# Kernel tuning notes

Measured on AMD Instinct MI355X. Metric: run time of the kernel, lower is better.

The kernel has to match this reference:

```python
import jax, jax.numpy as jnp
import numpy as np

H = 16          # n_heads
DH = 128        # head_dim
DR = 64         # rope_dim
DC = DH - DR    # content_dim = 64
THETA = 10000.0
SCALE = 1.0 / np.sqrt(DH)


def _rope_tables(T, dtype):
    inv = 1.0 / (THETA ** (jnp.arange(0, DR, 2, dtype=jnp.float32) / DR))  # [DR/2]
    t = jnp.arange(T, dtype=jnp.float32)
    freqs = jnp.outer(t, inv)  # [T, DR/2]
    return jnp.cos(freqs).astype(dtype), jnp.sin(freqs).astype(dtype)


def _apply_rope(x, cos, sin):
    # x: [B,H,T,DR]; cos/sin: [T,DR/2] broadcast over B,H
    d = x.shape[-1] // 2
    x1, x2 = x[..., :d], x[..., d:]
    return jnp.concatenate([x1 * cos - x2 * sin, x1 * sin + x2 * cos], axis=-1)


def setup_inputs() -> dict:
    key = jax.random.key(0)
    ks = jax.random.split(key, 9)
    B, T, D = 1, 2048, 2048
    s = 0.02
    return {
        "x": jax.random.normal(ks[0], (B, T, D), jnp.float32),
        "Wq_down": jax.random.normal(ks[1], (D, 512), jnp.float32) * s,
        "Wq_up": jax.random.normal(ks[2], (512, H * DC), jnp.float32) * s,
        "Wq_rope": jax.random.normal(ks[3], (D, H * DR), jnp.float32) * s,
        "Wkv_down": jax.random.normal(ks[4], (D, 512), jnp.float32) * s,
        "Wk_up": jax.random.normal(ks[5], (512, H * DC), jnp.float32) * s,
        "Wv_up": jax.random.normal(ks[6], (512, H * DH), jnp.float32) * s,
        "Wk_rope": jax.random.normal(ks[7], (D, H * DR), jnp.float32) * s,
        "Wo": jax.random.normal(ks[8], (H * DH, D), jnp.float32) * s,
    }


def reference(x, Wq_down, Wq_up, Wq_rope, Wkv_down, Wk_up, Wv_up, Wk_rope, Wo):
    B, T, D = x.shape
    # low-rank query path: down then up, content part only
    q_content = ((x @ Wq_down) @ Wq_up).reshape(B, T, H, DC).transpose(0, 2, 1, 3)
    q_pos = (x @ Wq_rope).reshape(B, T, H, DR).transpose(0, 2, 1, 3)
    kv_latent = x @ Wkv_down                    # [B,T,d_latent]
    k_pos = (x @ Wk_rope).reshape(B, T, H, DR).transpose(0, 2, 1, 3)

    cos, sin = _rope_tables(T, x.dtype)
    q_pos = _apply_rope(q_pos, cos, sin)
    k_pos = _apply_rope(k_pos, cos, sin)

    k_content = (kv_latent @ Wk_up).reshape(B, T, H, DC).transpose(0, 2, 1, 3)
    v = (kv_latent @ Wv_up).reshape(B, T, H, DH).transpose(0, 2, 1, 3)

    q = jnp.concatenate([q_content, q_pos], axis=-1)  # [B,H,T,DH]
    k = jnp.concatenate([k_content, k_pos], axis=-1)  # [B,H,T,DH]

    scores = jnp.einsum("bhtd,bhsd->bhts", q, k) * SCALE
    causal = jnp.tril(jnp.ones((T, T), dtype=bool))
    scores = jnp.where(causal, scores, jnp.finfo(scores.dtype).min)
    attn = jax.nn.softmax(scores, axis=-1)
    out = jnp.einsum("bhts,bhsd->bhtd", attn, v)       # [B,H,T,DH]
    out = out.transpose(0, 2, 1, 3).reshape(B, T, H * DH)
    return out @ Wo
```

## Files before the change

kernel.cpp:

```cpp
#include <hip/hip_runtime.h>
#include <math.h>

#define T_SEQ 2048
#define D_MODEL 2048
#define H_HEADS 16
#define DH 128
#define DR 64
#define DC 64
#define D_LAT 512
#define SEGLEN 7
#define NSEG_TOT 46
#define NSEG_OF(q) ((2 * (q) + 2 + SEGLEN - 1) / SEGLEN)
#define QSCALE (0.08838834764831845f * 1.4426950408889634f)

typedef __attribute__((ext_vector_type(8))) short short8;
typedef __attribute__((ext_vector_type(4))) short short4v;
typedef __attribute__((ext_vector_type(4))) float f32x4;

#if __has_builtin(__builtin_amdgcn_exp2f)
#define EXP2(x) __builtin_amdgcn_exp2f(x)
#else
#define EXP2(x) exp2f(x)
#endif

__device__ __forceinline__ float bf2f(short b) {
    unsigned u = ((unsigned)(unsigned short)b) << 16;
    return __builtin_bit_cast(float, u);
}
__device__ __forceinline__ short f2bf(float f) {
    unsigned u = __builtin_bit_cast(unsigned, f);
    unsigned r = u + 0x7fffu + ((u >> 16) & 1u);
    return (short)(r >> 16);
}
__device__ __forceinline__ unsigned f2bf_tru(float f) {
    return __builtin_bit_cast(unsigned, f) >> 16;
}

#define GLD_LDS(gp, lp) \
    __builtin_amdgcn_global_load_lds( \
        (const __attribute__((address_space(1))) void*)(gp), \
        (__attribute__((address_space(3))) void*)(lp), 16, 0, 0)

__device__ __forceinline__ void ct_tile(float (*tile)[33],
                                        const float* __restrict__ W,
                                        short* __restrict__ Wt,
                                        int R, int C, int ldo, int rel) {
    int bx = rel % (C / 32), by = rel / (C / 32);
    int c0 = bx * 32, r0 = by * 32;
    int tx = threadIdx.x & 31, ty = threadIdx.x >> 5;
    #pragma unroll
    for (int i = 0; i < 4; ++i)
        tile[ty + i * 8][tx] = W[(size_t)(r0 + ty + i * 8) * C + c0 + tx];
    __syncthreads();
    #pragma unroll
    for (int i = 0; i < 4; ++i)
        Wt[(size_t)(c0 + ty + i * 8) * ldo + r0 + tx] = f2bf(tile[tx][ty + i * 8]);
    __syncthreads();
}

__global__ __launch_bounds__(256) void prep(const float* __restrict__ x,
                                            short* __restrict__ xb,
                                            const float* __restrict__ Wqd,
                                            const float* __restrict__ Wkvd,
                                            const float* __restrict__ Wqr,
                                            const float* __restrict__ Wkr,
                                            const float* __restrict__ Wqu,
                                            const float* __restrict__ Wku,
                                            const float* __restrict__ Wvu,
                                            const float* __restrict__ Wo,
                                            short* __restrict__ WdT,
                                            short* __restrict__ WupT2,
                                            short* __restrict__ WoT) {
    __shared__ float tile[32][33];
    int bid = blockIdx.x;
    if (bid < 4096) {
        int i = bid * 1024 + threadIdx.x * 4;
        float4 f = *(const float4*)&x[i];
        short4v o;
        o.x = f2bf(f.x); o.y = f2bf(f.y); o.z = f2bf(f.z); o.w = f2bf(f.w);
        *(short4v*)&xb[i] = o;
    } else if (bid < 5120) {
        ct_tile(tile, Wqd,  WdT + (size_t)0 * 2048,    2048, 512,  2048, bid - 4096);
    } else if (bid < 6144) {
        ct_tile(tile, Wkvd, WdT + (size_t)512 * 2048,  2048, 512,  2048, bid - 5120);
    } else if (bid < 8192) {
        ct_tile(tile, Wqr,  WdT + (size_t)1024 * 2048, 2048, 1024, 2048, bid - 6144);
    } else if (bid < 10240) {
        ct_tile(tile, Wkr,  WdT + (size_t)2048 * 2048, 2048, 1024, 2048, bid - 8192);
    } else if (bid < 10752) {
        ct_tile(tile, Wqu,  WupT2 + (size_t)0 * 512,    512, 1024, 512, bid - 10240);
    } else if (bid < 11264) {
        ct_tile(tile, Wku,  WupT2 + (size_t)1024 * 512, 512, 1024, 512, bid - 10752);
    } else if (bid < 12288) {
        ct_tile(tile, Wvu,  WupT2 + (size_t)2048 * 512, 512, 2048, 512, bid - 11264);
    } else {
        ct_tile(tile, Wo,   WoT, 2048, 2048, 2048, bid - 12288);
    }
}

__global__ __launch_bounds__(256) void transpose_bf16(const short* __restrict__ in,
                                                      short* __restrict__ vTc,
                                                      int ldi) {
    __shared__ short tile[64][65];
    int c0 = blockIdx.x * 64, t0 = blockIdx.y * 64;
    int tx = threadIdx.x & 31, ty = threadIdx.x >> 5;
    #pragma unroll
    for (int i = 0; i < 8; ++i) {
        int r = ty + i * 8;
        int vv = *(const int*)&in[(size_t)(t0 + r) * ldi + c0 + tx * 2];
        tile[r][tx * 2]     = (short)(vv & 0xffff);
        tile[r][tx * 2 + 1] = (short)(((unsigned)vv) >> 16);
    }
    __syncthreads();
    #pragma unroll
    for (int i = 0; i < 8; ++i) {
        int G = i * 256 + threadIdx.x;
        int ch2 = G >> 10;
        int rem = G & 1023;
        int dl = rem >> 4;
        int mp = rem & 15;
        int dval = c0 + dl;
        int h = dval >> 7, d128 = dval & 127;
        int kl = 4 * ((mp >> 2) ^ (d128 & 3)) + (mp & 3);
        unsigned lo = (unsigned short)tile[ch2 * 32 + kl][dl];
        unsigned hi = (unsigned short)tile[ch2 * 32 + kl + 16][dl];
        int chg = (t0 >> 5) + ch2;
        size_t off = ((size_t)(h * 64 + chg)) * 4096 + d128 * 32 + mp * 2;
        *(int*)&vTc[off] = (int)(lo | (hi << 16));
    }
}

__global__ __launch_bounds__(256) void gemm_bt(const short* __restrict__ A,
                                               const short* __restrict__ A2,
                                               const short* __restrict__ Bt,
                                               short* __restrict__ C0,
                                               short* __restrict__ C1,
                                               short* __restrict__ C2,
                                               short* __restrict__ C3,
                                               int N, int Kblk,
                                               int lda, int ldb, int ldc,
                                               int ncut, int scut, float cscale) {
    __shared__ short As[128 * 32];
    __shared__ short Bs[128 * 32];
    const int tid = threadIdx.x;
    const int wave = tid >> 6, lane = tid & 63;
    const int lin = blockIdx.x;
    const int X = N >> 7, Xq = X >> 2;
    const int xcd = lin & 7;
    int r = lin >> 3;
    const int bx = (xcd & 3) * Xq + (r % Xq); r /= Xq;
    const int by = (xcd >> 2) * 8 + (r & 7);
    const int bz = r >> 3;
    const int row0 = by * 128, col0 = bx * 128;
    const int kbase = bz * Kblk;
    const short* Ause = (col0 < ncut) ? A : A2;
    short* Cuse = (bz == 0) ? C0 : (bz == 1) ? C1 : (bz == 2) ? C2 : C3;
    const int wr = (wave >> 1) * 64, wc = (wave & 1) * 64;
    const int lr = lane & 15, quad = lane >> 4;

    f32x4 acc[4][4];
    #pragma unroll
    for (int i = 0; i < 4; ++i)
        #pragma unroll
        for (int j = 0; j < 4; ++j) acc[i][j] = (f32x4){0.f, 0.f, 0.f, 0.f};

    for (int k0 = kbase; k0 < kbase + Kblk; k0 += 32) {
        __syncthreads();
        #pragma unroll
        for (int it = 0; it < 2; ++it) {
            int idx = wave * 64 + it * 256 + lane;
            const short* ga = Ause + (size_t)(row0 + (idx >> 2)) * lda + k0 + (idx & 3) * 8;
            const short* gb = Bt   + (size_t)(col0 + (idx >> 2)) * ldb + k0 + (idx & 3) * 8;
            int lds0 = (wave * 64 + it * 256) * 8;
            GLD_LDS(ga, &As[lds0]);
            GLD_LDS(gb, &Bs[lds0]);
        }
        __syncthreads();

        short8 af[4], bfr[4];
        #pragma unroll
        for (int i = 0; i < 4; ++i)
            af[i] = *(const short8*)&As[(wr + i * 16 + lr) * 32 + quad * 8];
        #pragma unroll
        for (int j = 0; j < 4; ++j)
            bfr[j] = *(const short8*)&Bs[(wc + j * 16 + lr) * 32 + quad * 8];
        #pragma unroll
        for (int i = 0; i < 4; ++i)
            #pragma unroll
            for (int j = 0; j < 4; ++j)
                acc[i][j] = __builtin_amdgcn_mfma_f32_16x16x32_bf16(af[i], bfr[j],
                                                                   acc[i][j], 0, 0, 0);
    }

    const float sc = (col0 < scut) ? cscale : 1.0f;
    #pragma unroll
    for (int i = 0; i < 4; ++i) {
        int rb = row0 + wr + i * 16 + quad * 4;
        #pragma unroll
        for (int j = 0; j < 4; ++j) {
            int c = col0 + wc + j * 16 + lr;
            #pragma unroll
            for (int rr = 0; rr < 4; ++rr)
                Cuse[(size_t)(rb + rr) * ldc + c] = f2bf(acc[i][j][rr] * sc);
        }
    }
}

__global__ __launch_bounds__(192) void finish_down(short* __restrict__ cat,
                                                   const short* __restrict__ pdown) {
    const int t = blockIdx.x;
    const int k8 = threadIdx.x * 8;
    const int c0 = ((k8 >> 5) << 6) + (k8 & 31);
    const size_t lo = (size_t)t * 3072 + c0;
    const size_t hi = lo + 32;
    short8 al = *(const short8*)&cat[lo];
    short8 ah = *(const short8*)&cat[hi];
    short8 bl = *(const short8*)&pdown[lo];
    short8 bh = *(const short8*)&pdown[hi];
    float xl[8], xh[8];
    #pragma unroll
    for (int j = 0; j < 8; ++j) {
        xl[j] = bf2f(al[j]) + bf2f(bl[j]);
        xh[j] = bf2f(ah[j]) + bf2f(bh[j]);
    }
    if (c0 >= 1024) {
        float sc = (c0 < 2048) ? QSCALE : 1.0f;
        #pragma unroll
        for (int j = 0; j < 8; ++j) {
            int i = (c0 & 31) + j;
            float freq = (float)t * __powf(10000.0f, -(float)i / 32.0f);
            float cs = __cosf(freq), sn = __sinf(freq);
            float r1 = (xl[j] * cs - xh[j] * sn) * sc;
            float r2 = (xl[j] * sn + xh[j] * cs) * sc;
            xl[j] = r1; xh[j] = r2;
        }
    }
    short8 ol, oh;
    #pragma unroll
    for (int j = 0; j < 8; ++j) { ol[j] = f2bf(xl[j]); oh[j] = f2bf(xh[j]); }
    *(short8*)&cat[lo] = ol;
    *(short8*)&cat[hi] = oh;
}

__global__ __launch_bounds__(256) void add_out_f32(const short* __restrict__ p0,
                                                   const short* __restrict__ p1,
                                                   float* __restrict__ out) {
    int i = (blockIdx.x * 256 + threadIdx.x) * 4;
    short4v a = *(const short4v*)&p0[i];
    short4v b = *(const short4v*)&p1[i];
    float4 o;
    o.x = bf2f(a.x) + bf2f(b.x);
    o.y = bf2f(a.y) + bf2f(b.y);
    o.z = bf2f(a.z) + bf2f(b.z);
    o.w = bf2f(a.w) + bf2f(b.w);
    *(float4*)&out[i] = o;
}

__global__ __launch_bounds__(256) void attn_mla_split(const short* __restrict__ qkup,
                                                      const short* __restrict__ cat,
                                                      const short* __restrict__ vTc,
                                                      short* __restrict__ slabA,
                                                      short* __restrict__ slabB,
                                                      float* __restrict__ lpart) {
    const int lin = blockIdx.x;
    const int xcd = lin & 7;
    int k_ = lin >> 3;
    const int h = xcd + 8 * (k_ & 1);
    const int pp = k_ >> 1;
    int qt = 0, s = 0, acc = 0;
    #pragma unroll
    for (int q = 0; q < 16; ++q) {
        const int ns = NSEG_OF(q);
        if (pp >= acc) { qt = q; s = pp - acc; }
        acc += ns;
    }
    const int nchunk = 2 * qt + 2;
    const int nsq = NSEG_OF(qt);
    const int cbase = nchunk / nsq, crem = nchunk % nsq;
    const int c0 = s * cbase + (s < crem ? s : crem);
    const int c1 = c0 + cbase + (s < crem ? 1 : 0);

    const int tid = threadIdx.x;
    const int wave = tid >> 6, lane = tid & 63;
    const int lr = lane & 15, quad = lane >> 4;

    __shared__ short Ks[2][32 * 128];
    __shared__ short Vst[2][128 * 32];
    __shared__ short Ps[4][2][16 * 40];

    const short8 ones = {0x3F80, 0x3F80, 0x3F80, 0x3F80,
                         0x3F80, 0x3F80, 0x3F80, 0x3F80};

    const int Q0 = qt * 128;
    const int qrowA = Q0 + wave * 16;
    const int qrowB = qrowA + 64;

    short8 qf[2][4];
    #pragma unroll
    for (int sb = 0; sb < 2; ++sb) {
        int t = (sb ? qrowB : qrowA) + lr;
        #pragma unroll
        for (int kci = 0; kci < 4; ++kci) {
            const short* src = (kci < 2)
                ? qkup + (size_t)t * 4096 + h * 64
                : cat + (size_t)t * 3072 + 1024 + h * 64;
            qf[sb][kci] = *(const short8*)&src[(kci & 1) * 32 + quad * 8];
        }
    }

    const int idx = wave * 64 + lane;
    const int key = idx >> 4;
    const int cg = (idx & 15) ^ (key & 15);
    const short* kp0 = (cg < 8)
        ? qkup + (size_t)key * 4096 + 1024 + h * 64 + cg * 8
        : cat + (size_t)key * 3072 + 2048 + h * 64 + (cg - 8) * 8;
    const int kst = (cg < 8) ? 4096 : 3072;
    const short* kp1 = kp0 + (size_t)16 * kst;
    const short* vp0 = vTc + ((size_t)h * 64 + (size_t)c0 * 2) * 4096 + idx * 8;
    kp0 += (size_t)c0 * 64 * kst; kp1 += (size_t)c0 * 64 * kst;
    const int kadv = 64 * kst;
    const int kph = 32 * kst;
    const int ldsA = (wave * 64) * 8;
    const int ldsB = (wave * 64 + 256) * 8;

    f32x4 Oacc[2][8];
    #pragma unroll
    for (int sb = 0; sb < 2; ++sb)
        #pragma unroll
        for (int d = 0; d < 8; ++d) Oacc[sb][d] = (f32x4){0.f, 0.f, 0.f, 0.f};
    f32x4 Lacc[2];
    Lacc[0] = (f32x4){0.f, 0.f, 0.f, 0.f};
    Lacc[1] = (f32x4){0.f, 0.f, 0.f, 0.f};

    for (int cc = c0; cc < c1; ++cc) {
        __syncthreads();
        GLD_LDS(kp0,        &Ks[0][ldsA]);
        GLD_LDS(kp1,        &Ks[0][ldsB]);
        GLD_LDS(kp0 + kph,  &Ks[1][ldsA]);
        GLD_LDS(kp1 + kph,  &Ks[1][ldsB]);
        GLD_LDS(vp0,        &Vst[0][ldsA]);
        GLD_LDS(vp0 + 2048, &Vst[0][ldsB]);
        GLD_LDS(vp0 + 4096, &Vst[1][ldsA]);
        GLD_LDS(vp0 + 6144, &Vst[1][ldsB]);
        kp0 += kadv; kp1 += kadv; vp0 += 8192;
        __syncthreads();

        #pragma unroll
        for (int half = 0; half < 2; ++half) {
            const int s0 = cc * 64 + half * 32;
            if (s0 > qrowB + 15) continue;
            const bool actA = (s0 <= qrowA + 15);
            const short* Kc = Ks[half];
            const short* Vc = Vst[half];

            f32x4 sacc[2][2];
            #pragma unroll
            for (int sb = 0; sb < 2; ++sb)
                #pragma unroll
                for (int n = 0; n < 2; ++n) sacc[sb][n] = (f32x4){0.f, 0.f, 0.f, 0.f};
            #pragma unroll
            for (int n = 0; n < 2; ++n) {
                #pragma unroll
                for (int kci = 0; kci < 4; ++kci) {
                    short8 kf = *(const short8*)
                        &Kc[(n * 16 + lr) * 128 + ((kci * 4 + quad) ^ lr) * 8];
                    if (actA)
                        sacc[0][n] = __builtin_amdgcn_mfma_f32_16x16x32_bf16(
                            qf[0][kci], kf, sacc[0][n], 0, 0, 0);
                    sacc[1][n] = __builtin_amdgcn_mfma_f32_16x16x32_bf16(
                        qf[1][kci], kf, sacc[1][n], 0, 0, 0);
                }
            }
            #pragma unroll
            for (int sb = 0; sb < 2; ++sb) {
                if (sb == 0 && !actA) continue;
                const int qrow0 = sb ? qrowB : qrowA;
                if (s0 + 31 > qrow0) {
                    #pragma unroll
                    for (int r = 0; r < 4; ++r) {
                        int qg = qrow0 + quad * 4 + r;
                        #pragma unroll
                        for (int n = 0; n < 2; ++n) {
                            int sidx = s0 + n * 16 + lr;
                            sacc[sb][n][r] = (sidx <= qg) ? sacc[sb][n][r] : -1e30f;
                        }
                    }
                }
                #pragma unroll
                for (int r = 0; r < 4; ++r) {
                    unsigned pk = f2bf_tru(EXP2(sacc[sb][0][r])) |
                                  (f2bf_tru(EXP2(sacc[sb][1][r])) << 16);
                    *(unsigned*)&Ps[wave][sb][(quad * 4 + r) * 40 + lr * 2] = pk;
                }
            }
            short8 pfA, pfB;
            if (actA) {
                pfA = *(const short8*)&Ps[wave][0][lr * 40 + quad * 8];
                Lacc[0] = __builtin_amdgcn_mfma_f32_16x16x32_bf16(pfA, ones,
                                                                  Lacc[0], 0, 0, 0);
            }
            pfB = *(const short8*)&Ps[wave][1][lr * 40 + quad * 8];
            Lacc[1] = __builtin_amdgcn_mfma_f32_16x16x32_bf16(pfB, ones,
                                                              Lacc[1], 0, 0, 0);
            #pragma unroll
            for (int dt = 0; dt < 8; ++dt) {
                short8 vf = *(const short8*)
                    &Vc[(dt * 16 + lr) * 32 + (quad ^ (lr & 3)) * 8];
                if (actA)
                    Oacc[0][dt] = __builtin_amdgcn_mfma_f32_16x16x32_bf16(
                        pfA, vf, Oacc[0][dt], 0, 0, 0);
                Oacc[1][dt] = __builtin_amdgcn_mfma_f32_16x16x32_bf16(
                    pfB, vf, Oacc[1][dt], 0, 0, 0);
            }
        }
    }

    const int slot = h * NSEG_TOT + pp;
    short* slotp = (slot < 512) ? slabA + (size_t)slot * 16384
                                : slabB + (size_t)(slot - 512) * 16384;
    #pragma unroll
    for (int sb = 0; sb < 2; ++sb) {
        const int rbase = wave * 16 + sb * 64 + quad * 4;
        #pragma unroll
        for (int r = 0; r < 4; ++r) {
            #pragma unroll
            for (int dt = 0; dt < 8; ++dt)
                slotp[(rbase + r) * 128 + dt * 16 + lr] = f2bf(Oacc[sb][dt][r]);
        }
        if (lr == 0) {
            #pragma unroll
            for (int r = 0; r < 4; ++r)
                lpart[(size_t)slot * 128 + rbase + r] = Lacc[sb][r];
        }
    }
}

__global__ __launch_bounds__(256) void attn_combine(const short* __restrict__ slabA,
                                                    const short* __restrict__ slabB,
                                                    const float* __restrict__ lpart,
                                                    short* __restrict__ ao) {
    const int t = blockIdx.x;
    const int qt = t >> 7, rl = t & 127;
    const int h = threadIdx.x >> 4;
    const int di = (threadIdx.x & 15) * 8;
    int pf = 0;
    #pragma unroll
    for (int q = 0; q < 16; ++q)
        if (q < qt) pf += NSEG_OF(q);
    const int ns = NSEG_OF(qt);
    float o[8] = {0.f, 0.f, 0.f, 0.f, 0.f, 0.f, 0.f, 0.f};
    float den = 0.f;
    for (int s = 0; s < ns; ++s) {
        const int slot = h * NSEG_TOT + pf + s;
        const short* sp = (slot < 512) ? slabA + (size_t)slot * 16384
                                       : slabB + (size_t)(slot - 512) * 16384;
        short8 v = *(const short8*)&sp[rl * 128 + di];
        #pragma unroll
        for (int j = 0; j < 8; ++j) o[j] += bf2f(v[j]);
        den += lpart[(size_t)slot * 128 + rl];
    }
    float inv = 1.0f / den;
    short8 ov;
    #pragma unroll
    for (int j = 0; j < 8; ++j) ov[j] = f2bf(o[j] * inv);
    *(short8*)&ao[(size_t)t * 2048 + h * 128 + di] = ov;
}

extern "C" void kernel_launch(void* const* d_in, const int* in_sizes, int n_in,
                              void* d_out, int out_size, void* d_ws, size_t ws_size,
                              hipStream_t stream) {
    const float* x        = (const float*)d_in[0];
    const float* Wq_down  = (const float*)d_in[1];
    const float* Wq_up    = (const float*)d_in[2];
    const float* Wq_rope  = (const float*)d_in[3];
    const float* Wkv_down = (const float*)d_in[4];
    const float* Wk_up    = (const float*)d_in[5];
    const float* Wv_up    = (const float*)d_in[6];
    const float* Wk_rope  = (const float*)d_in[7];
    const float* Wo       = (const float*)d_in[8];
    float* out = (float*)d_out;

    short* p = (short*)d_ws;
    short* xb     = p; p += (size_t)2048 * 2048;
    short* WoT    = p; p += (size_t)2048 * 2048;
    short* cat    = p; p += (size_t)2048 * 3072;
    short* upcat2 = p; p += (size_t)2048 * 4096;
    short* WdT    = p; p += (size_t)3072 * 2048;
    short* WupT2  = p; p += (size_t)4096 * 512;
    short* vTc    = p; p += (size_t)2048 * 2048;
    float* lpart  = (float*)p;
    short* pdown   = upcat2;
    short* aob     = cat;
    short* slabA   = WdT;
    short* slabB   = xb;
    short* pw0     = upcat2;
    short* pw1     = upcat2 + (size_t)2048 * 2048;

    prep<<<dim3(16384), 256, 0, stream>>>(x, xb, Wq_down, Wkv_down, Wq_rope,
                                          Wk_rope, Wq_up, Wk_up, Wv_up, Wo,
                                          WdT, WupT2, WoT);

    gemm_bt<<<dim3(24 * 16 * 2), 256, 0, stream>>>(xb, xb, WdT, cat, pdown,
                                                   nullptr, nullptr,
                                                   3072, 1024,
                                                   2048, 2048, 3072, 1 << 30, 0, 1.f);

    finish_down<<<dim3(2048), 192, 0, stream>>>(cat, pdown);

    gemm_bt<<<dim3(32 * 16 * 1), 256, 0, stream>>>(cat, cat + 512, WupT2,
                                                   upcat2, nullptr, nullptr, nullptr,
                                                   4096, 512,
                                                   3072, 512, 4096, 1024, 1024, QSCALE);

    transpose_bf16<<<dim3(32, 32), 256, 0, stream>>>(upcat2 + 2048, vTc, 4096);

    attn_mla_split<<<dim3(16 * NSEG_TOT), 256, 0, stream>>>(upcat2, cat, vTc,
                                                            slabA, slabB, lpart);
    attn_combine<<<dim3(2048), 256, 0, stream>>>(slabA, slabB, lpart, aob);

    gemm_bt<<<dim3(16 * 16 * 2), 256, 0, stream>>>(aob, aob, WoT, pw0, pw1,
                                                   nullptr, nullptr,
                                                   2048, 1024,
                                                   2048, 2048, 2048, 1 << 30, 0, 1.f);
    add_out_f32<<<dim3(2048 * 2048 / 1024), 256, 0, stream>>>(pw0, pw1, out);
}
```

Measured before the change: 272.1 us.

## Replace split-KV attention plus combine with single-pass per-tile attention

Drops the split-KV decomposition (46 segments per head plus a separate combine kernel) and has each block process a full query tile over all causal key chunks, normalizing and writing the output directly. Heaviest tiles are scheduled first (qt = 15 - index) so the uneven causal work balances better. This removes the slab write/read traffic, the lpart buffer and one kernel launch. The cost is only 256 blocks on a 256-CU device, so parallelism drops and the longest tile sets the critical path.

After: 303.1 us. +11.4%, slower.

```diff
diff --git a/kernel.cpp b/kernel.cpp
--- a/kernel.cpp
+++ b/kernel.cpp
@@ -8,9 +8,6 @@
 #define DR 64
 #define DC 64
 #define D_LAT 512
-#define SEGLEN 7
-#define NSEG_TOT 46
-#define NSEG_OF(q) ((2 * (q) + 2 + SEGLEN - 1) / SEGLEN)
 #define QSCALE (0.08838834764831845f * 1.4426950408889634f)
 
 typedef __attribute__((ext_vector_type(8))) short short8;
@@ -256,29 +253,16 @@
     *(float4*)&out[i] = o;
 }
 
-__global__ __launch_bounds__(256) void attn_mla_split(const short* __restrict__ qkup,
-                                                      const short* __restrict__ cat,
-                                                      const short* __restrict__ vTc,
-                                                      short* __restrict__ slabA,
-                                                      short* __restrict__ slabB,
-                                                      float* __restrict__ lpart) {
+__global__ __launch_bounds__(256) void attn_mla(const short* __restrict__ qkup,
+                                                const short* __restrict__ cat,
+                                                const short* __restrict__ vTc,
+                                                short* __restrict__ ao) {
     const int lin = blockIdx.x;
     const int xcd = lin & 7;
-    int k_ = lin >> 3;
-    const int h = xcd + 8 * (k_ & 1);
-    const int pp = k_ >> 1;
-    int qt = 0, s = 0, acc = 0;
-    #pragma unroll
-    for (int q = 0; q < 16; ++q) {
-        const int ns = NSEG_OF(q);
-        if (pp >= acc) { qt = q; s = pp - acc; }
-        acc += ns;
-    }
+    const int r_ = lin >> 3;
+    const int h = xcd + 8 * (r_ & 1);
+    const int qt = 15 - (r_ >> 1);
     const int nchunk = 2 * qt + 2;
-    const int nsq = NSEG_OF(qt);
-    const int cbase = nchunk / nsq, crem = nchunk % nsq;
-    const int c0 = s * cbase + (s < crem ? s : crem);
-    const int c1 = c0 + cbase + (s < crem ? 1 : 0);
 
     const int tid = threadIdx.x;
     const int wave = tid >> 6, lane = tid & 63;
@@ -316,8 +300,7 @@
         : cat + (size_t)key * 3072 + 2048 + h * 64 + (cg - 8) * 8;
     const int kst = (cg < 8) ? 4096 : 3072;
     const short* kp1 = kp0 + (size_t)16 * kst;
-    const short* vp0 = vTc + ((size_t)h * 64 + (size_t)c0 * 2) * 4096 + idx * 8;
-    kp0 += (size_t)c0 * 64 * kst; kp1 += (size_t)c0 * 64 * kst;
+    const short* vp0 = vTc + (size_t)h * 64 * 4096 + idx * 8;
     const int kadv = 64 * kst;
     const int kph = 32 * kst;
     const int ldsA = (wave * 64) * 8;
@@ -332,7 +315,7 @@
     Lacc[0] = (f32x4){0.f, 0.f, 0.f, 0.f};
     Lacc[1] = (f32x4){0.f, 0.f, 0.f, 0.f};
 
-    for (int cc = c0; cc < c1; ++cc) {
+    for (int cc = 0; cc < nchunk; ++cc) {
         __syncthreads();
         GLD_LDS(kp0,        &Ks[0][ldsA]);
         GLD_LDS(kp1,        &Ks[0][ldsB]);
@@ -415,55 +398,19 @@
         }
     }
 
-    const int slot = h * NSEG_TOT + pp;
-    short* slotp = (slot < 512) ? slabA + (size_t)slot * 16384
-                                : slabB + (size_t)(slot - 512) * 16384;
     #pragma unroll
     for (int sb = 0; sb < 2; ++sb) {
-        const int rbase = wave * 16 + sb * 64 + quad * 4;
+        const int qrow0 = sb ? qrowB : qrowA;
         #pragma unroll
         for (int r = 0; r < 4; ++r) {
+            const int t = qrow0 + quad * 4 + r;
+            const float inv = 1.0f / Lacc[sb][r];
             #pragma unroll
             for (int dt = 0; dt < 8; ++dt)
-                slotp[(rbase + r) * 128 + dt * 16 + lr] = f2bf(Oacc[sb][dt][r]);
-        }
-        if (lr == 0) {
-            #pragma unroll
-            for (int r = 0; r < 4; ++r)
-                lpart[(size_t)slot * 128 + rbase + r] = Lacc[sb][r];
-        }
-    }
-}
-
-__global__ __launch_bounds__(256) void attn_combine(const short* __restrict__ slabA,
-                                                    const short* __restrict__ slabB,
-                                                    const float* __restrict__ lpart,
-                                                    short* __restrict__ ao) {
-    const int t = blockIdx.x;
-    const int qt = t >> 7, rl = t & 127;
-    const int h = threadIdx.x >> 4;
-    const int di = (threadIdx.x & 15) * 8;
-    int pf = 0;
-    #pragma unroll
-    for (int q = 0; q < 16; ++q)
-        if (q < qt) pf += NSEG_OF(q);
-    const int ns = NSEG_OF(qt);
-    float o[8] = {0.f, 0.f, 0.f, 0.f, 0.f, 0.f, 0.f, 0.f};
-    float den = 0.f;
-    for (int s = 0; s < ns; ++s) {
-        const int slot = h * NSEG_TOT + pf + s;
-        const short* sp = (slot < 512) ? slabA + (size_t)slot * 16384
-                                       : slabB + (size_t)(slot - 512) * 16384;
-        short8 v = *(const short8*)&sp[rl * 128 + di];
-        #pragma unroll
-        for (int j = 0; j < 8; ++j) o[j] += bf2f(v[j]);
-        den += lpart[(size_t)slot * 128 + rl];
-    }
-    float inv = 1.0f / den;
-    short8 ov;
-    #pragma unroll
-    for (int j = 0; j < 8; ++j) ov[j] = f2bf(o[j] * inv);
-    *(short8*)&ao[(size_t)t * 2048 + h * 128 + di] = ov;
+                ao[(size_t)t * 2048 + h * 128 + dt * 16 + lr] =
+                    f2bf(Oacc[sb][dt][r] * inv);
+        }
+    }
 }
 
 extern "C" void kernel_launch(void* const* d_in, const int* in_sizes, int n_in,
@@ -488,11 +435,8 @@
     short* WdT    = p; p += (size_t)3072 * 2048;
     short* WupT2  = p; p += (size_t)4096 * 512;
     short* vTc    = p; p += (size_t)2048 * 2048;
-    float* lpart  = (float*)p;
     short* pdown   = upcat2;
-    short* aob     = cat;
-    short* slabA   = WdT;
-    short* slabB   = xb;
+    short* aob     = WdT;
     short* pw0     = upcat2;
     short* pw1     = upcat2 + (size_t)2048 * 2048;
 
@@ -514,9 +458,7 @@
 
     transpose_bf16<<<dim3(32, 32), 256, 0, stream>>>(upcat2 + 2048, vTc, 4096);
 
-    attn_mla_split<<<dim3(16 * NSEG_TOT), 256, 0, stream>>>(upcat2, cat, vTc,
-                                                            slabA, slabB, lpart);
-    attn_combine<<<dim3(2048), 256, 0, stream>>>(slabA, slabB, lpart, aob);
+    attn_mla<<<dim3(256), 256, 0, stream>>>(upcat2, cat, vTc, aob);
 
     gemm_bt<<<dim3(16 * 16 * 2), 256, 0, stream>>>(aob, aob, WoT, pw0, pw1,
                                                    nullptr, nullptr,
```
